# Kernel tuning notes

Measured on AMD Instinct MI355X. Metric: run time of the kernel, lower is better.

## Reference

```python
import jax, jax.numpy as jnp
import numpy as np

N_NODES = 100000
N_EDGES = 1600000
IN_DIM, HID_DIM, OUT_DIM = 256, 128, 32
NEG_SLOPE = 0.2  # GATConv default negative_slope


def setup_inputs() -> dict:
    key = jax.random.key(0)
    ks = jax.random.split(key, 6)
    x = jax.random.normal(ks[0], (N_NODES, IN_DIM), dtype=jnp.float32)
    edge_index = jax.random.randint(ks[1], (2, N_EDGES), 0, N_NODES, dtype=jnp.int64)
    # conv1: lin_src [in, hid], att_src/att_dst [hid] (heads=1)
    W1 = jax.random.normal(ks[2], (IN_DIM, HID_DIM), dtype=jnp.float32) * 0.05
    a1_src = jax.random.normal(ks[3], (HID_DIM,), dtype=jnp.float32) * 0.05
    a1_dst = jax.random.normal(ks[4], (HID_DIM,), dtype=jnp.float32) * 0.05
    # conv2: lin_src [hid, out]; conv2 runs with attention=False so no att params needed
    W2 = jax.random.normal(ks[5], (HID_DIM, OUT_DIM), dtype=jnp.float32) * 0.05
    return {"x": x, "W1": W1, "a1_src": a1_src, "a1_dst": a1_dst, "W2": W2,
            "edge_index": edge_index}


def _gat_aggregate(xs, alpha_src, alpha_dst, src, dst, n):
    """Segment-softmax attention aggregation (heads=1).
    xs: [N,C] transformed features; alpha_src/alpha_dst: [N] per-node logits.
    Edge e: j=src[e] -> i=dst[e]; softmax over edges grouped by dst."""
    e = jax.nn.leaky_relu(alpha_src[src] + alpha_dst[dst], NEG_SLOPE)  # [E]
    m = jax.ops.segment_max(e, dst, num_segments=n)                    # [N]
    w = jnp.exp(e - m[dst])                                            # [E]
    s = jax.ops.segment_sum(w, dst, num_segments=n)                    # [N]
    a = w / s[dst]                                                     # [E]
    return jax.ops.segment_sum(xs[src] * a[:, None], dst, num_segments=n)


def reference(x, W1, a1_src, a1_dst, W2, edge_index):
    src, dst = edge_index[0], edge_index[1]
    n = x.shape[0]

    # conv1 (attention=True): also caches per-node attention logits (tied later)
    xs1 = x @ W1                       # [N, hid]
    as1 = xs1 @ a1_src                 # [N]
    ad1 = xs1 @ a1_dst                 # [N]
    h1 = jax.nn.elu(_gat_aggregate(xs1, as1, ad1, src, dst, n))

    # conv2 (attention=False): returns x @ lin_src (heads=1, concat=False)
    h2 = h1 @ W2                       # [N, out]

    # conv3: weights tied to W2^T, attention tied to conv1's logits
    xs3 = h2 @ W2.T                    # [N, hid]
    h3 = jax.nn.elu(_gat_aggregate(xs3, as1, ad1, src, dst, n))

    # conv4 (attention=False): weights tied to W1^T
    h4 = h3 @ W1.T                     # [N, in]

    return (h2, h4)
```

## Files before the change

### kernel.cpp

```cpp
#include <hip/hip_runtime.h>
#include <math.h>

#define IN_DIM 256
#define HID 128
#define OUTD 32
#define NEG_SLOPE 0.2f
#define BSH 8
#define EPB 4096

typedef unsigned short ushort_t;
typedef unsigned int uint_t;
typedef __attribute__((ext_vector_type(8))) short short8;
typedef __attribute__((ext_vector_type(4))) float f32x4;

__device__ __forceinline__ ushort_t f2b(float f) {
    union { float f; uint_t i; } v; v.f = f;
    uint_t x = v.i;
    uint_t r = (x + 0x7FFFu + ((x >> 16) & 1u)) >> 16;
    return (ushort_t)r;
}

__device__ __forceinline__ float b2f(ushort_t b) {
    union { uint_t i; float f; } v; v.i = ((uint_t)b) << 16;
    return v.f;
}

__global__ __launch_bounds__(256) void swz_kernel(
    const float* __restrict__ W1, const float* __restrict__ W2,
    ushort_t* __restrict__ W1B, ushort_t* __restrict__ W1TB, ushort_t* __restrict__ W2TB)
{
    int idx = blockIdx.x * 256 + threadIdx.x;
    if (idx < 32768) {
        int j = idx & 7, l = (idx >> 3) & 63, t = (idx >> 9) & 7, s = idx >> 12;
        int n = 16 * t + (l & 15), k = 32 * s + (l >> 4) * 8 + j;
        W1B[idx] = f2b(W1[k * HID + n]);
    } else if (idx < 65536) {
        int o = idx - 32768;
        int j = o & 7, l = (o >> 3) & 63, t = (o >> 9) & 15, s = o >> 13;
        int n = 16 * t + (l & 15), k = 32 * s + (l >> 4) * 8 + j;
        W1TB[o] = f2b(W1[n * HID + k]);
    } else if (idx < 69632) {
        int o = idx - 65536;
        int j = o & 7, l = (o >> 3) & 63, t = o >> 9;
        int n = 16 * t + (l & 15), k = (l >> 4) * 8 + j;
        W2TB[o] = f2b(W2[n * OUTD + k]);
    }
}

__global__ __launch_bounds__(256) void gemm1_mfma(
    const float* __restrict__ x, const ushort_t* __restrict__ W1B,
    const float* __restrict__ a_src, const float* __restrict__ a_dst,
    ushort_t* __restrict__ xs1b, float* __restrict__ as1, float* __restrict__ ad1, int N)
{
    __shared__ ushort_t lx[64 * 264];
    const int tid = threadIdx.x;
    const int row0 = blockIdx.x * 64;
    const int nrows = min(64, N - row0);

    for (int i = tid; i < nrows * 32; i += 256) {
        int r = i >> 5, c = i & 31;
        const float* p = x + (size_t)(row0 + r) * IN_DIM + c * 8;
        float4 v0 = *(const float4*)p;
        float4 v1 = *(const float4*)(p + 4);
        ushort_t o[8] = { f2b(v0.x), f2b(v0.y), f2b(v0.z), f2b(v0.w),
                          f2b(v1.x), f2b(v1.y), f2b(v1.z), f2b(v1.w) };
        *(uint4*)(&lx[r * 264 + c * 8]) = *(uint4*)o;
    }
    __syncthreads();

    const int wave = tid >> 6, lane = tid & 63;
    const int lo = lane & 15, q = lane >> 4;
    f32x4 acc[8];
    #pragma unroll
    for (int t = 0; t < 8; t++) acc[t] = (f32x4){0.f, 0.f, 0.f, 0.f};

    const int arow = wave * 16 + lo;
    #pragma unroll
    for (int s = 0; s < 8; s++) {
        short8 af = *(const short8*)(&lx[arow * 264 + s * 32 + q * 8]);
        #pragma unroll
        for (int t = 0; t < 8; t++) {
            short8 bf = *(const short8*)(W1B + ((size_t)(s * 8 + t) * 64 + lane) * 8);
            acc[t] = __builtin_amdgcn_mfma_f32_16x16x32_bf16(af, bf, acc[t], 0, 0, 0);
        }
    }

    float asv[8], adv[8];
    #pragma unroll
    for (int t = 0; t < 8; t++) { asv[t] = a_src[t * 16 + lo]; adv[t] = a_dst[t * 16 + lo]; }
    #pragma unroll
    for (int r = 0; r < 4; r++) {
        float vs = 0.f, vd = 0.f;
        #pragma unroll
        for (int t = 0; t < 8; t++) { vs += acc[t][r] * asv[t]; vd += acc[t][r] * adv[t]; }
        #pragma unroll
        for (int off = 1; off < 16; off <<= 1) {
            vs += __shfl_xor(vs, off, 64);
            vd += __shfl_xor(vd, off, 64);
        }
        int m = row0 + wave * 16 + q * 4 + r;
        if (lo == 0 && m < N) { as1[m] = vs; ad1[m] = vd; }
    }

    #pragma unroll
    for (int r = 0; r < 4; r++) {
        int m = row0 + wave * 16 + q * 4 + r;
        if (m < N) {
            #pragma unroll
            for (int t = 0; t < 8; t++)
                xs1b[(size_t)m * HID + t * 16 + lo] = f2b(acc[t][r]);
        }
    }
}

__global__ __launch_bounds__(256) void gemm3g_mfma(
    const ushort_t* __restrict__ gb, const ushort_t* __restrict__ W2TB,
    ushort_t* __restrict__ h3b, int N)
{
    __shared__ ushort_t lh[64 * 40];
    const int tid = threadIdx.x;
    const int row0 = blockIdx.x * 64;
    const int nrows = min(64, N - row0);
    for (int i = tid; i < nrows * 4; i += 256) {
        int r = i >> 2, c = i & 3;
        *(uint4*)(&lh[r * 40 + c * 8]) =
            *(const uint4*)(gb + (size_t)(row0 + r) * OUTD + c * 8);
    }
    __syncthreads();

    const int wave = tid >> 6, lane = tid & 63;
    const int lo = lane & 15, q = lane >> 4;
    f32x4 acc[8];
    #pragma unroll
    for (int t = 0; t < 8; t++) acc[t] = (f32x4){0.f, 0.f, 0.f, 0.f};
    short8 af = *(const short8*)(&lh[(wave * 16 + lo) * 40 + q * 8]);
    #pragma unroll
    for (int t = 0; t < 8; t++) {
        short8 bf = *(const short8*)(W2TB + ((size_t)t * 64 + lane) * 8);
        acc[t] = __builtin_amdgcn_mfma_f32_16x16x32_bf16(af, bf, acc[t], 0, 0, 0);
    }
    #pragma unroll
    for (int r = 0; r < 4; r++) {
        int m = row0 + wave * 16 + q * 4 + r;
        if (m < N) {
            #pragma unroll
            for (int t = 0; t < 8; t++) {
                float v = acc[t][r];
                v = v > 0.f ? v : expm1f(v);
                h3b[(size_t)m * HID + t * 16 + lo] = f2b(v);
            }
        }
    }
}

__global__ __launch_bounds__(256) void gemm4_mfma(
    const ushort_t* __restrict__ h3b, const ushort_t* __restrict__ W1TB,
    float* __restrict__ h4, int N)
{
    __shared__ ushort_t lh[64 * 136];
    const int tid = threadIdx.x;
    const int row0 = blockIdx.x * 64;
    const int nrows = min(64, N - row0);
    for (int i = tid; i < nrows * 16; i += 256) {
        int r = i >> 4, c = i & 15;
        *(uint4*)(&lh[r * 136 + c * 8]) =
            *(const uint4*)(h3b + (size_t)(row0 + r) * HID + c * 8);
    }
    __syncthreads();

    const int wave = tid >> 6, lane = tid & 63;
    const int lo = lane & 15, q = lane >> 4;
    f32x4 acc[16];
    #pragma unroll
    for (int t = 0; t < 16; t++) acc[t] = (f32x4){0.f, 0.f, 0.f, 0.f};
    const int arow = wave * 16 + lo;
    #pragma unroll
    for (int s = 0; s < 4; s++) {
        short8 af = *(const short8*)(&lh[arow * 136 + s * 32 + q * 8]);
        #pragma unroll
        for (int t = 0; t < 16; t++) {
            short8 bf = *(const short8*)(W1TB + ((size_t)(s * 16 + t) * 64 + lane) * 8);
            acc[t] = __builtin_amdgcn_mfma_f32_16x16x32_bf16(af, bf, acc[t], 0, 0, 0);
        }
    }
    #pragma unroll
    for (int r = 0; r < 4; r++) {
        int m = row0 + wave * 16 + q * 4 + r;
        if (m < N) {
            #pragma unroll
            for (int t = 0; t < 16; t++)
                h4[(size_t)m * IN_DIM + t * 16 + lo] = acc[t][r];
        }
    }
}

__global__ __launch_bounds__(256) void bhist_kernel(
    const int* __restrict__ dst, int* __restrict__ bcnt, int E, int B)
{
    __shared__ int lcnt[512];
    int t = threadIdx.x;
    for (int i = t; i < B; i += 256) lcnt[i] = 0;
    __syncthreads();
    int base = blockIdx.x * EPB;
    int end = min(base + EPB, E);
    for (int e = base + t; e < end; e += 256)
        atomicAdd(&lcnt[dst[e] >> BSH], 1);
    __syncthreads();
    for (int i = t; i < B; i += 256) {
        int c = lcnt[i];
        if (c) atomicAdd(&bcnt[i], c);
    }
}

__global__ __launch_bounds__(512) void bscan_kernel(
    const int* __restrict__ bcnt, int* __restrict__ boff, int* __restrict__ gcur,
    int* __restrict__ off, int B, int N, int E)
{
    __shared__ int l[512];
    int t = threadIdx.x;
    int v = (t < B) ? bcnt[t] : 0;
    l[t] = v;
    __syncthreads();
    for (int o = 1; o < 512; o <<= 1) {
        int u = (t >= o) ? l[t - o] : 0;
        __syncthreads();
        l[t] += u;
        __syncthreads();
    }
    int pre = l[t] - v;
    if (t < B) { boff[t] = pre; gcur[t] = pre; }
    if (t == B - 1) boff[B] = pre + v;
    if (t == 0) off[N] = E;
}

__global__ __launch_bounds__(256) void bscatter_kernel(
    const int* __restrict__ src, const int* __restrict__ dst,
    int* __restrict__ gcur, int2* __restrict__ barr, int E, int B)
{
    __shared__ int lpos[512];
    int t = threadIdx.x;
    for (int i = t; i < B; i += 256) lpos[i] = 0;
    __syncthreads();
    int base = blockIdx.x * EPB;
    int end = min(base + EPB, E);
    for (int e = base + t; e < end; e += 256)
        atomicAdd(&lpos[dst[e] >> BSH], 1);
    __syncthreads();
    for (int i = t; i < B; i += 256) {
        int c = lpos[i];
        if (c) lpos[i] = atomicAdd(&gcur[i], c);
    }
    __syncthreads();
    for (int e = base + t; e < end; e += 256) {
        int s = src[e], d = dst[e];
        int p = atomicAdd(&lpos[d >> BSH], 1);
        barr[p] = make_int2(s, d);
    }
}

__global__ __launch_bounds__(256) void bsort_kernel(
    const int2* __restrict__ barr, const int* __restrict__ boff,
    const float* __restrict__ as1, const float* __restrict__ ad1,
    int* __restrict__ off, int2* __restrict__ epk, int N)
{
    __shared__ int ldeg[256];
    __shared__ int lscan[256];
    __shared__ float lsum[256];
    int b = blockIdx.x, t = threadIdx.x;
    int d0 = b << BSH;
    int e0 = boff[b], e1 = boff[b + 1];
    ldeg[t] = 0;
    lsum[t] = 0.f;
    __syncthreads();
    for (int e = e0 + t; e < e1; e += 256)
        atomicAdd(&ldeg[barr[e].y & 255], 1);
    __syncthreads();
    int my = ldeg[t];
    lscan[t] = my;
    __syncthreads();
    for (int o = 1; o < 256; o <<= 1) {
        int u = (t >= o) ? lscan[t - o] : 0;
        __syncthreads();
        lscan[t] += u;
        __syncthreads();
    }
    int pre = lscan[t] - my;
    int d = d0 + t;
    if (d < N) off[d] = e0 + pre;
    ldeg[t] = pre;
    __syncthreads();
    for (int e = e0 + t; e < e1; e += 256) {
        int2 r = barr[e];
        float v = as1[r.x] + ad1[r.y];
        v = v > 0.f ? v : NEG_SLOPE * v;
        float w = __expf(v);
        int p = atomicAdd(&ldeg[r.y & 255], 1);
        epk[e0 + p] = make_int2(r.x, __float_as_int(w));
        atomicAdd(&lsum[r.y & 255], w);
    }
    __syncthreads();
    float s = lsum[t];
    float inv = (my > 0 && s > 0.f) ? 1.0f / s : 0.f;
    int base = e0 + pre;
    for (int i = 0; i < my; i++) {
        int2 r = epk[base + i];
        epk[base + i] = make_int2(r.x, __float_as_int(__int_as_float(r.y) * inv));
    }
}

__global__ __launch_bounds__(256) void agg128_kernel(
    const ushort_t* __restrict__ xsb, const int* __restrict__ off,
    const int2* __restrict__ epk, float* __restrict__ outf, int N)
{
    int d = blockIdx.x * 4 + (threadIdx.x >> 6);
    if (d >= N) return;
    const int lane = threadIdx.x & 63;
    const int g = lane >> 4, li = lane & 15;
    const int e0 = off[d], e1 = off[d + 1];

    float acc[8];
    #pragma unroll
    for (int j = 0; j < 8; j++) acc[j] = 0.f;

    int e = e0 + g;
    for (; e + 4 < e1; e += 8) {
        int2 p0 = epk[e], p1 = epk[e + 4];
        float w0 = __int_as_float(p0.y), w1 = __int_as_float(p1.y);
        uint4 u0 = *(const uint4*)(xsb + (size_t)p0.x * HID + li * 8);
        uint4 u1 = *(const uint4*)(xsb + (size_t)p1.x * HID + li * 8);
        acc[0] += w0 * __uint_as_float(u0.x << 16)        + w1 * __uint_as_float(u1.x << 16);
        acc[1] += w0 * __uint_as_float(u0.x & 0xFFFF0000u) + w1 * __uint_as_float(u1.x & 0xFFFF0000u);
        acc[2] += w0 * __uint_as_float(u0.y << 16)        + w1 * __uint_as_float(u1.y << 16);
        acc[3] += w0 * __uint_as_float(u0.y & 0xFFFF0000u) + w1 * __uint_as_float(u1.y & 0xFFFF0000u);
        acc[4] += w0 * __uint_as_float(u0.z << 16)        + w1 * __uint_as_float(u1.z << 16);
        acc[5] += w0 * __uint_as_float(u0.z & 0xFFFF0000u) + w1 * __uint_as_float(u1.z & 0xFFFF0000u);
        acc[6] += w0 * __uint_as_float(u0.w << 16)        + w1 * __uint_as_float(u1.w << 16);
        acc[7] += w0 * __uint_as_float(u0.w & 0xFFFF0000u) + w1 * __uint_as_float(u1.w & 0xFFFF0000u);
    }
    if (e < e1) {
        int2 p0 = epk[e];
        float w0 = __int_as_float(p0.y);
        uint4 u0 = *(const uint4*)(xsb + (size_t)p0.x * HID + li * 8);
        acc[0] += w0 * __uint_as_float(u0.x << 16);
        acc[1] += w0 * __uint_as_float(u0.x & 0xFFFF0000u);
        acc[2] += w0 * __uint_as_float(u0.y << 16);
        acc[3] += w0 * __uint_as_float(u0.y & 0xFFFF0000u);
        acc[4] += w0 * __uint_as_float(u0.z << 16);
        acc[5] += w0 * __uint_as_float(u0.z & 0xFFFF0000u);
        acc[6] += w0 * __uint_as_float(u0.w << 16);
        acc[7] += w0 * __uint_as_float(u0.w & 0xFFFF0000u);
    }

    #pragma unroll
    for (int j = 0; j < 8; j++) {
        acc[j] += __shfl_xor(acc[j], 16, 64);
        acc[j] += __shfl_xor(acc[j], 32, 64);
    }
    if (g != 0) return;
    float o[8];
    #pragma unroll
    for (int j = 0; j < 8; j++) {
        float v = acc[j];
        o[j] = v > 0.f ? v : expm1f(v);
    }
    float4 o0 = make_float4(o[0], o[1], o[2], o[3]);
    float4 o1 = make_float4(o[4], o[5], o[6], o[7]);
    *(float4*)(outf + (size_t)d * HID + li * 8) = o0;
    *(float4*)(outf + (size_t)d * HID + li * 8 + 4) = o1;
}

__global__ __launch_bounds__(256) void agg32_kernel(
    const ushort_t* __restrict__ h2b, const int* __restrict__ off,
    const int2* __restrict__ epk, ushort_t* __restrict__ gb, int N)
{
    int d = blockIdx.x * 4 + (threadIdx.x >> 6);
    if (d >= N) return;
    const int lane = threadIdx.x & 63;
    const int g = lane >> 2, li = lane & 3;
    const int e0 = off[d], e1 = off[d + 1];

    float acc[8];
    #pragma unroll
    for (int j = 0; j < 8; j++) acc[j] = 0.f;

    for (int e = e0 + g; e < e1; e += 16) {
        int2 p = epk[e];
        float w = __int_as_float(p.y);
        uint4 u = *(const uint4*)(h2b + (size_t)p.x * OUTD + li * 8);
        acc[0] += w * __uint_as_float(u.x << 16);
        acc[1] += w * __uint_as_float(u.x & 0xFFFF0000u);
        acc[2] += w * __uint_as_float(u.y << 16);
        acc[3] += w * __uint_as_float(u.y & 0xFFFF0000u);
        acc[4] += w * __uint_as_float(u.z << 16);
        acc[5] += w * __uint_as_float(u.z & 0xFFFF0000u);
        acc[6] += w * __uint_as_float(u.w << 16);
        acc[7] += w * __uint_as_float(u.w & 0xFFFF0000u);
    }

    #pragma unroll
    for (int j = 0; j < 8; j++) {
        acc[j] += __shfl_xor(acc[j], 4, 64);
        acc[j] += __shfl_xor(acc[j], 8, 64);
        acc[j] += __shfl_xor(acc[j], 16, 64);
        acc[j] += __shfl_xor(acc[j], 32, 64);
    }
    if (g != 0) return;
    ushort_t ob[8] = { f2b(acc[0]), f2b(acc[1]), f2b(acc[2]), f2b(acc[3]),
                       f2b(acc[4]), f2b(acc[5]), f2b(acc[6]), f2b(acc[7]) };
    *(uint4*)(gb + (size_t)d * OUTD + li * 8) = *(uint4*)ob;
}

__global__ __launch_bounds__(256) void gemm2_kernel(
    const float* __restrict__ h1, const float* __restrict__ W2,
    float* __restrict__ h2, ushort_t* __restrict__ h2b, int N)
{
    __shared__ float lh[32 * 129];
    const int tid = threadIdx.x;
    const int row0 = blockIdx.x * 32;
    const int nrows = min(32, N - row0);
    for (int i = tid; i < nrows * 32; i += 256) {
        int r = i >> 5, q = i & 31;
        float4 v = *(const float4*)(h1 + (size_t)(row0 + r) * HID + q * 4);
        float* d = &lh[r * 129 + q * 4];
        d[0] = v.x; d[1] = v.y; d[2] = v.z; d[3] = v.w;
    }
    __syncthreads();
    const int r = tid >> 3;
    const int c0 = (tid & 7) * 4;
    float a0 = 0, a1 = 0, a2 = 0, a3 = 0;
    for (int k = 0; k < HID; k++) {
        float h = lh[r * 129 + k];
        float4 w = *(const float4*)(W2 + k * OUTD + c0);
        a0 += h * w.x; a1 += h * w.y; a2 += h * w.z; a3 += h * w.w;
    }
    if (r < nrows) {
        float4 o; o.x = a0; o.y = a1; o.z = a2; o.w = a3;
        *(float4*)(h2 + (size_t)(row0 + r) * OUTD + c0) = o;
        ushort_t ob[4] = { f2b(a0), f2b(a1), f2b(a2), f2b(a3) };
        *(uint2*)(h2b + (size_t)(row0 + r) * OUTD + c0) = *(uint2*)ob;
    }
}

extern "C" void kernel_launch(void* const* d_in, const int* in_sizes, int n_in,
                              void* d_out, int out_size, void* d_ws, size_t ws_size,
                              hipStream_t stream)
{
    const float* x     = (const float*)d_in[0];
    const float* W1    = (const float*)d_in[1];
    const float* a_src = (const float*)d_in[2];
    const float* a_dst = (const float*)d_in[3];
    const float* W2    = (const float*)d_in[4];
    const int*   ei    = (const int*)d_in[5];

    const int N = in_sizes[0] / IN_DIM;
    const int E = in_sizes[5] / 2;
    const int* src = ei;
    const int* dst = ei + E;
    const int B = (N + 255) >> BSH;

    float* ws = (float*)d_ws;
    size_t o = 0;
    ushort_t* A   = (ushort_t*)(ws + o); o += (size_t)N * HID / 2;
    float* Bb  = ws + o; o += (size_t)N * HID;
    float* as1 = ws + o; o += N;
    float* ad1 = ws + o; o += N;
    ushort_t* h3b  = (ushort_t*)(ws + o); o += (size_t)N * HID / 2;
    ushort_t* h2b  = (ushort_t*)(ws + o); o += (size_t)N * OUTD / 2;
    ushort_t* W1B  = (ushort_t*)(ws + o); o += 16384;
    ushort_t* W1TB = (ushort_t*)(ws + o); o += 16384;
    ushort_t* W2TB = (ushort_t*)(ws + o); o += 2048;
    int2* barr = (int2*)(ws + o); o += (size_t)E * 2;
    int2* epk  = (int2*)(ws + o); o += (size_t)E * 2;
    int* off  = (int*)(ws + o);
    int* bcnt = off + N + 1;
    int* boff = bcnt + B;
    int* gcur = boff + B + 1;

    float* h2 = (float*)d_out;
    float* h4 = h2 + (size_t)N * OUTD;

    hipMemsetAsync(bcnt, 0, (size_t)B * sizeof(int), stream);

    swz_kernel<<<(69632 + 255) / 256, 256, 0, stream>>>(W1, W2, W1B, W1TB, W2TB);

    gemm1_mfma<<<(N + 63) / 64, 256, 0, stream>>>(x, W1B, a_src, a_dst, A, as1, ad1, N);

    const int GB = (E + EPB - 1) / EPB;
    bhist_kernel<<<GB, 256, 0, stream>>>(dst, bcnt, E, B);
    bscan_kernel<<<1, 512, 0, stream>>>(bcnt, boff, gcur, off, B, N, E);
    bscatter_kernel<<<GB, 256, 0, stream>>>(src, dst, gcur, barr, E, B);
    bsort_kernel<<<B, 256, 0, stream>>>(barr, boff, as1, ad1, off, epk, N);

    agg128_kernel<<<(N + 3) / 4, 256, 0, stream>>>(A, off, epk, Bb, N);
    gemm2_kernel<<<(N + 31) / 32, 256, 0, stream>>>(Bb, W2, h2, h2b, N);

    ushort_t* gb = A;
    agg32_kernel<<<(N + 3) / 4, 256, 0, stream>>>(h2b, off, epk, gb, N);
    gemm3g_mfma<<<(N + 63) / 64, 256, 0, stream>>>(gb, W2TB, h3b, N);
    gemm4_mfma<<<(N + 63) / 64, 256, 0, stream>>>(h3b, W1TB, h4, N);
}
```

Before: 505.4 us.

## Defer softmax normalization to aggregation and use bf16 dot2 for edge pairs

Removes the serial per-thread renormalization pass over edges in bsort by storing a per-node reciprocal sum, which the aggregation kernels apply once to the accumulated result. agg128 now processes adjacent edge pairs per group and uses the bf16 fdot2 instruction with packed bf16 weights, which cuts VALU work. Rounding the attention weights to bf16 lowers their precision. The edge-pairing order changes memory access locality.

```diff
diff --git a/kernel.cpp b/kernel.cpp
--- a/kernel.cpp
+++ b/kernel.cpp
@@ -12,6 +12,13 @@
 typedef unsigned int uint_t;
 typedef __attribute__((ext_vector_type(8))) short short8;
 typedef __attribute__((ext_vector_type(4))) float f32x4;
+typedef __attribute__((ext_vector_type(2))) __bf16 bf16x2;
+
+#if defined(__has_builtin)
+#if __has_builtin(__builtin_amdgcn_fdot2_f32_bf16)
+#define USE_DOT2 1
+#endif
+#endif
 
 __device__ __forceinline__ ushort_t f2b(float f) {
     union { float f; uint_t i; } v; v.f = f;
@@ -261,7 +268,7 @@
 __global__ __launch_bounds__(256) void bsort_kernel(
     const int2* __restrict__ barr, const int* __restrict__ boff,
     const float* __restrict__ as1, const float* __restrict__ ad1,
-    int* __restrict__ off, int2* __restrict__ epk, int N)
+    int* __restrict__ off, int2* __restrict__ epk, float* __restrict__ winv, int N)
 {
     __shared__ int ldeg[256];
     __shared__ int lscan[256];
@@ -299,32 +306,59 @@
         atomicAdd(&lsum[r.y & 255], w);
     }
     __syncthreads();
-    float s = lsum[t];
-    float inv = (my > 0 && s > 0.f) ? 1.0f / s : 0.f;
-    int base = e0 + pre;
-    for (int i = 0; i < my; i++) {
-        int2 r = epk[base + i];
-        epk[base + i] = make_int2(r.x, __float_as_int(__int_as_float(r.y) * inv));
+    if (d < N) {
+        float s = lsum[t];
+        winv[d] = (my > 0 && s > 0.f) ? 1.0f / s : 0.f;
     }
 }
 
 __global__ __launch_bounds__(256) void agg128_kernel(
     const ushort_t* __restrict__ xsb, const int* __restrict__ off,
-    const int2* __restrict__ epk, float* __restrict__ outf, int N)
+    const int2* __restrict__ epk, const float* __restrict__ winv,
+    float* __restrict__ outf, int N)
 {
     int d = blockIdx.x * 4 + (threadIdx.x >> 6);
     if (d >= N) return;
     const int lane = threadIdx.x & 63;
     const int g = lane >> 4, li = lane & 15;
     const int e0 = off[d], e1 = off[d + 1];
+    const float wi = winv[d];
 
     float acc[8];
     #pragma unroll
     for (int j = 0; j < 8; j++) acc[j] = 0.f;
 
-    int e = e0 + g;
-    for (; e + 4 < e1; e += 8) {
-        int2 p0 = epk[e], p1 = epk[e + 4];
+    int e = e0 + 2 * g;
+#ifdef USE_DOT2
+    for (; e + 1 < e1; e += 8) {
+        int2 p0 = epk[e], p1 = epk[e + 1];
+        uint_t wpair;
+        asm("v_cvt_pk_bf16_f32 %0, %1, %2"
+            : "=v"(wpair)
+            : "v"(__int_as_float(p0.y)), "v"(__int_as_float(p1.y)));
+        bf16x2 wp = __builtin_bit_cast(bf16x2, wpair);
+        uint4 u0 = *(const uint4*)(xsb + (size_t)p0.x * HID + li * 8);
+        uint4 u1 = *(const uint4*)(xsb + (size_t)p1.x * HID + li * 8);
+        acc[0] = __builtin_amdgcn_fdot2_f32_bf16(
+            __builtin_bit_cast(bf16x2, __builtin_amdgcn_perm(u0.x, u1.x, 0x01000504u)), wp, acc[0], false);
+        acc[1] = __builtin_amdgcn_fdot2_f32_bf16(
+            __builtin_bit_cast(bf16x2, __builtin_amdgcn_perm(u0.x, u1.x, 0x03020706u)), wp, acc[1], false);
+        acc[2] = __builtin_amdgcn_fdot2_f32_bf16(
+            __builtin_bit_cast(bf16x2, __builtin_amdgcn_perm(u0.y, u1.y, 0x01000504u)), wp, acc[2], false);
+        acc[3] = __builtin_amdgcn_fdot2_f32_bf16(
+            __builtin_bit_cast(bf16x2, __builtin_amdgcn_perm(u0.y, u1.y, 0x03020706u)), wp, acc[3], false);
+        acc[4] = __builtin_amdgcn_fdot2_f32_bf16(
+            __builtin_bit_cast(bf16x2, __builtin_amdgcn_perm(u0.z, u1.z, 0x01000504u)), wp, acc[4], false);
+        acc[5] = __builtin_amdgcn_fdot2_f32_bf16(
+            __builtin_bit_cast(bf16x2, __builtin_amdgcn_perm(u0.z, u1.z, 0x03020706u)), wp, acc[5], false);
+        acc[6] = __builtin_amdgcn_fdot2_f32_bf16(
+            __builtin_bit_cast(bf16x2, __builtin_amdgcn_perm(u0.w, u1.w, 0x01000504u)), wp, acc[6], false);
+        acc[7] = __builtin_amdgcn_fdot2_f32_bf16(
+            __builtin_bit_cast(bf16x2, __builtin_amdgcn_perm(u0.w, u1.w, 0x03020706u)), wp, acc[7], false);
+    }
+#else
+    for (; e + 1 < e1; e += 8) {
+        int2 p0 = epk[e], p1 = epk[e + 1];
         float w0 = __int_as_float(p0.y), w1 = __int_as_float(p1.y);
         uint4 u0 = *(const uint4*)(xsb + (size_t)p0.x * HID + li * 8);
         uint4 u1 = *(const uint4*)(xsb + (size_t)p1.x * HID + li * 8);
@@ -337,6 +371,7 @@
         acc[6] += w0 * __uint_as_float(u0.w << 16)        + w1 * __uint_as_float(u1.w << 16);
         acc[7] += w0 * __uint_as_float(u0.w & 0xFFFF0000u) + w1 * __uint_as_float(u1.w & 0xFFFF0000u);
     }
+#endif
     if (e < e1) {
         int2 p0 = epk[e];
         float w0 = __int_as_float(p0.y);
@@ -360,7 +395,7 @@
     float o[8];
     #pragma unroll
     for (int j = 0; j < 8; j++) {
-        float v = acc[j];
+        float v = acc[j] * wi;
         o[j] = v > 0.f ? v : expm1f(v);
     }
     float4 o0 = make_float4(o[0], o[1], o[2], o[3]);
@@ -371,13 +406,15 @@
 
 __global__ __launch_bounds__(256) void agg32_kernel(
     const ushort_t* __restrict__ h2b, const int* __restrict__ off,
-    const int2* __restrict__ epk, ushort_t* __restrict__ gb, int N)
+    const int2* __restrict__ epk, const float* __restrict__ winv,
+    ushort_t* __restrict__ gb, int N)
 {
     int d = blockIdx.x * 4 + (threadIdx.x >> 6);
     if (d >= N) return;
     const int lane = threadIdx.x & 63;
     const int g = lane >> 2, li = lane & 3;
     const int e0 = off[d], e1 = off[d + 1];
+    const float wi = winv[d];
 
     float acc[8];
     #pragma unroll
@@ -405,8 +442,8 @@
         acc[j] += __shfl_xor(acc[j], 32, 64);
     }
     if (g != 0) return;
-    ushort_t ob[8] = { f2b(acc[0]), f2b(acc[1]), f2b(acc[2]), f2b(acc[3]),
-                       f2b(acc[4]), f2b(acc[5]), f2b(acc[6]), f2b(acc[7]) };
+    ushort_t ob[8] = { f2b(acc[0] * wi), f2b(acc[1] * wi), f2b(acc[2] * wi), f2b(acc[3] * wi),
+                       f2b(acc[4] * wi), f2b(acc[5] * wi), f2b(acc[6] * wi), f2b(acc[7] * wi) };
     *(uint4*)(gb + (size_t)d * OUTD + li * 8) = *(uint4*)ob;
 }
 
@@ -464,6 +501,7 @@
     float* Bb  = ws + o; o += (size_t)N * HID;
     float* as1 = ws + o; o += N;
     float* ad1 = ws + o; o += N;
+    float* winv = ws + o; o += N;
     ushort_t* h3b  = (ushort_t*)(ws + o); o += (size_t)N * HID / 2;
     ushort_t* h2b  = (ushort_t*)(ws + o); o += (size_t)N * OUTD / 2;
     ushort_t* W1B  = (ushort_t*)(ws + o); o += 16384;
@@ -489,13 +527,13 @@
     bhist_kernel<<<GB, 256, 0, stream>>>(dst, bcnt, E, B);
     bscan_kernel<<<1, 512, 0, stream>>>(bcnt, boff, gcur, off, B, N, E);
     bscatter_kernel<<<GB, 256, 0, stream>>>(src, dst, gcur, barr, E, B);
-    bsort_kernel<<<B, 256, 0, stream>>>(barr, boff, as1, ad1, off, epk, N);
-
-    agg128_kernel<<<(N + 3) / 4, 256, 0, stream>>>(A, off, epk, Bb, N);
+    bsort_kernel<<<B, 256, 0, stream>>>(barr, boff, as1, ad1, off, epk, winv, N);
+
+    agg128_kernel<<<(N + 3) / 4, 256, 0, stream>>>(A, off, epk, winv, Bb, N);
     gemm2_kernel<<<(N + 31) / 32, 256, 0, stream>>>(Bb, W2, h2, h2b, N);
 
     ushort_t* gb = A;
-    agg32_kernel<<<(N + 3) / 4, 256, 0, stream>>>(h2b, off, epk, gb, N);
+    agg32_kernel<<<(N + 3) / 4, 256, 0, stream>>>(h2b, off, epk, winv, gb, N);
     gemm3g_mfma<<<(N + 63) / 64, 256, 0, stream>>>(gb, W2TB, h3b, N);
     gemm4_mfma<<<(N + 63) / 64, 256, 0, stream>>>(h3b, W1TB, h4, N);
 }
```

After: 493.1 us. -2.4%, faster.
